# Kernel optimization log

Measured on AMD Instinct MI355X. Metric: run time of the kernel, lower is better.

## Reference

```python
import jax, jax.numpy as jnp
import numpy as np

DT = 0.01
REG = 0.01

def setup_inputs() -> dict:
    key = jax.random.key(0)
    k1, k2, k3, k4 = jax.random.split(key, 4)
    B, C_in, L = 16, 128, 4096
    C_out, KS = 256, 9
    return {
        "x": jax.random.normal(k1, (B, C_in, L), dtype=jnp.float32),
        "weight": jax.random.normal(k2, (C_out, C_in, KS), dtype=jnp.float32) * np.sqrt(2.0 / (C_out * KS)),
        "bias": jnp.zeros((C_out,), dtype=jnp.float32),
        "vel": jax.random.normal(k3, (C_in, KS), dtype=jnp.float32) * 0.1,
        "acc": jax.random.normal(k4, (C_in, KS), dtype=jnp.float32) * 0.01,
        "ks": 9,
        "stride": 1,
        "pad": 4,
    }

def reference(x, weight, bias, vel, acc, ks, stride, pad):
    # x: [B, C_in, L]
    if pad > 0:
        x = jnp.pad(x, ((0, 0), (0, 0), (pad, pad)), mode="edge")  # replicate pad
    L_pad = x.shape[2]
    L_out = (L_pad - ks) // stride + 1
    t_off = jnp.arange(ks, dtype=jnp.float32) * DT  # [ks]
    # unfold: gather sliding windows -> [B, C_in, L_out, ks]
    idx = jnp.arange(L_out)[:, None] * stride + jnp.arange(ks)[None, :]
    xu = x[:, :, idx]
    # per-tap physics offset: vel*t + 0.5*acc*t^2, shape [C_in, ks] broadcast
    offset = vel * t_off + 0.5 * acc * (t_off ** 2)  # [C_in, ks]
    xt = xu + offset[None, :, None, :]  # [B, C_in, L_out, ks]
    # GEMM: [B, L_out, C_in*ks] x [C_in*ks, C_out]
    out = jnp.einsum("bclk,ock->bol", xt, weight) + bias[None, :, None]
    phys = REG * (jnp.mean(vel ** 2) + jnp.mean(acc ** 2))
    return (out, phys)
```

## Files before the change

### kernel.cpp

```cpp
#include <hip/hip_runtime.h>
#include <hip/hip_bf16.h>

typedef unsigned short u16;
typedef __bf16 bf16x8 __attribute__((ext_vector_type(8)));
typedef float f32x4 __attribute__((ext_vector_type(4)));
typedef float f32x16 __attribute__((ext_vector_type(16)));
typedef unsigned short ushort8 __attribute__((ext_vector_type(8)));

#define C_IN   128
#define C_OUT  256
#define BATCH  16
#define LEN    4096
#define KS     9
#define PAD    4
#define LPAD   (LEN + 2*PAD)
#define KTOT   (C_IN * KS)
#define NSTEP  72

#define XT_BLKS    1040
#define W5_BLKS    1152
#define EB_BLKS    256

__device__ inline u16 f2bf(float f) {
    __hip_bfloat16 h = __float2bfloat16(f);
    return __builtin_bit_cast(u16, h);
}

__device__ __forceinline__ void g2l16(const void* g, void* l) {
    __builtin_amdgcn_global_load_lds(
        (const __attribute__((address_space(1))) void*)g,
        (__attribute__((address_space(3))) void*)l, 16, 0, 0);
}

__global__ void prep_all(const float* __restrict__ x, const float* __restrict__ w,
                         const float* __restrict__ bias, const float* __restrict__ vel,
                         const float* __restrict__ acc_in,
                         u16* __restrict__ xt, u16* __restrict__ w5,
                         float* __restrict__ ebias, float* __restrict__ phys_out) {
    int bid = blockIdx.x;
    int t = threadIdx.x;
    if (bid < XT_BLKS) {
        int b    = bid / 65;
        int lblk = bid % 65;
        int lane = t & 63;
        int jb   = t >> 6;
        int lp   = lblk * 64 + lane;
        if (lp >= LPAD) return;
        int l = lp - PAD;
        l = l < 0 ? 0 : (l > LEN - 1 ? LEN - 1 : l);
        const float* xb = x + (size_t)b * C_IN * LEN + l;
        u16* row = xt + ((size_t)b * LPAD + lp) * C_IN;
        int key = lp & 15;
        #pragma unroll
        for (int jj = 0; jj < 4; ++jj) {
            int cblk = jb * 4 + jj;
            ushort8 v;
            #pragma unroll
            for (int e = 0; e < 8; ++e)
                v[e] = f2bf(xb[(size_t)(cblk * 8 + e) * LEN]);
            int jstore = cblk ^ key;
            *reinterpret_cast<ushort8*>(row + jstore * 8) = v;
        }
        return;
    }
    if (bid < XT_BLKS + W5_BLKS) {
        int i = (bid - XT_BLKS) * 256 + t;
        int e    = i & 7;
        int lane = (i >> 3) & 63;
        int g    = (i >> 9) & 7;
        int s    = i >> 12;
        int o    = g * 32 + (lane & 31);
        int hi   = lane >> 5;
        int c    = (s & 7) * 16 + hi * 8 + e;
        int k    = s >> 3;
        w5[i] = f2bf(w[((size_t)o * C_IN + c) * KS + k]);
        return;
    }
    __shared__ float red[256];
    int o = bid - (XT_BLKS + W5_BLKS);
    float sum = 0.f;
    for (int i = t; i < KTOT; i += 256) {
        int k = i % KS;
        float tk = k * 0.01f;
        float off = vel[i] * tk + 0.5f * acc_in[i] * tk * tk;
        sum += off * w[(size_t)o * KTOT + i];
    }
    red[t] = sum;
    __syncthreads();
    for (int h = 128; h > 0; h >>= 1) {
        if (t < h) red[t] += red[t + h];
        __syncthreads();
    }
    if (t == 0) ebias[o] = bias[o] + red[0];

    if (o == 0) {
        __syncthreads();
        float pv = 0.f;
        for (int i = t; i < KTOT; i += 256) {
            float v = vel[i], a = acc_in[i];
            pv += v * v + a * a;
        }
        red[t] = pv;
        __syncthreads();
        for (int h = 128; h > 0; h >>= 1) {
            if (t < h) red[t] += red[t + h];
            __syncthreads();
        }
        if (t == 0) *phys_out = 0.01f * (red[0] / (float)KTOT);
    }
}

__global__ __launch_bounds__(256, 2) void conv_main(const u16* __restrict__ xt,
                                                    const u16* __restrict__ w5,
                                                    const float* __restrict__ ebias,
                                                    float* __restrict__ out) {
    __shared__ u16 ldsx[17408];
    __shared__ u16 ldsa[2][4096];

    int b     = blockIdx.y;
    int lbase = blockIdx.x * 128;
    int t     = threadIdx.x;
    int lane  = t & 63;
    int w     = t >> 6;
    int wm    = w >> 1;
    int wn    = w & 1;
    int l31   = lane & 31;
    int hi    = lane >> 5;

    {
        const u16* bsrc = xt + ((size_t)b * LPAD + lbase) * C_IN;
        #pragma unroll
        for (int j = 0; j < 8; ++j)
            g2l16(bsrc + (j * 256 + t) * 8, ldsx + (j * 256 + w * 64) * 8);
        if (t < 128)
            g2l16(bsrc + (2048 + t) * 8, ldsx + (2048 + w * 64) * 8);
        #pragma unroll
        for (int j = 0; j < 2; ++j)
            g2l16(w5 + (j * 256 + t) * 8, ldsa[0] + (j * 256 + w * 64) * 8);
    }
    asm volatile("s_waitcnt vmcnt(0)" ::: "memory");
    __builtin_amdgcn_s_barrier();

    f32x16 acc[4][2] = {};
    const char* ldsbase = reinterpret_cast<const char*>(ldsx);

    #define LOAD_A(BUF, AF)                                                      \
        {                                                                        \
            const u16* ab_ = ldsa[BUF] + ((wm * 4) * 64 + lane) * 8;             \
            _Pragma("unroll")                                                    \
            for (int mi = 0; mi < 4; ++mi)                                       \
                AF[mi] = *reinterpret_cast<const bf16x8*>(ab_ + mi * 512);       \
        }
    #define LOAD_B(S, BF)                                                        \
        {                                                                        \
            int k_ = (S) >> 3;                                                   \
            int sl_ = ((S) & 7) * 2 + hi;                                        \
            _Pragma("unroll")                                                    \
            for (int nj = 0; nj < 2; ++nj) {                                     \
                int row_  = wn * 64 + nj * 32 + l31 + k_;                        \
                int addr_ = row_ * 256 + ((sl_ ^ (row_ & 15)) << 4);             \
                BF[nj] = *reinterpret_cast<const bf16x8*>(ldsbase + addr_);      \
            }                                                                    \
        }
    #define STAGE_A(S, BUF)                                                      \
        {                                                                        \
            const u16* as_ = w5 + (size_t)(S) * 4096;                            \
            _Pragma("unroll")                                                    \
            for (int j = 0; j < 2; ++j)                                          \
                g2l16(as_ + (j * 256 + t) * 8, ldsa[BUF] + (j * 256 + w * 64) * 8); \
        }
    #define MFMA8(AF, BF)                                                        \
        {                                                                        \
            _Pragma("unroll")                                                    \
            for (int mi = 0; mi < 4; ++mi)                                       \
                _Pragma("unroll")                                                \
                for (int nj = 0; nj < 2; ++nj)                                   \
                    acc[mi][nj] = __builtin_amdgcn_mfma_f32_32x32x16_bf16(       \
                        AF[mi], BF[nj], acc[mi][nj], 0, 0, 0);                   \
        }

    bf16x8 aA[4], aB[4], bA[2], bB[2];
    LOAD_B(0, bA);

    #pragma unroll
    for (int s = 0; s < NSTEP; s += 2) {
        STAGE_A(s + 1, 1);
        LOAD_A(0, aA);
        LOAD_B(s + 1, bB);
        MFMA8(aA, bA);
        asm volatile("s_waitcnt vmcnt(0) lgkmcnt(0)" ::: "memory");
        __builtin_amdgcn_s_barrier();
        if (s + 2 < NSTEP) STAGE_A(s + 2, 0);
        LOAD_A(1, aB);
        if (s + 2 < NSTEP) LOAD_B(s + 2, bA);
        MFMA8(aB, bB);
        if (s + 2 < NSTEP) {
            asm volatile("s_waitcnt vmcnt(0) lgkmcnt(0)" ::: "memory");
            __builtin_amdgcn_s_barrier();
        }
    }

    #pragma unroll
    for (int mi = 0; mi < 4; ++mi) {
        #pragma unroll
        for (int nj = 0; nj < 2; ++nj) {
            int o0 = wm * 128 + mi * 32 + hi * 4;
            int l  = lbase + wn * 64 + nj * 32 + l31;
            #pragma unroll
            for (int q = 0; q < 4; ++q) {
                f32x4 eb = *reinterpret_cast<const f32x4*>(ebias + o0 + q * 8);
                float* op = out + (size_t)(b * C_OUT + o0 + q * 8) * LEN + l;
                #pragma unroll
                for (int p = 0; p < 4; ++p)
                    op[(size_t)p * LEN] = acc[mi][nj][q * 4 + p] + eb[p];
            }
        }
    }
    #undef LOAD_A
    #undef LOAD_B
    #undef STAGE_A
    #undef MFMA8
}

extern "C" void kernel_launch(void* const* d_in, const int* in_sizes, int n_in,
                              void* d_out, int out_size, void* d_ws, size_t ws_size,
                              hipStream_t stream) {
    const float* x      = (const float*)d_in[0];
    const float* weight = (const float*)d_in[1];
    const float* bias   = (const float*)d_in[2];
    const float* vel    = (const float*)d_in[3];
    const float* acc    = (const float*)d_in[4];
    float* out = (float*)d_out;

    char* ws = (char*)d_ws;
    u16*  xt    = (u16*)ws;
    u16*  w5    = (u16*)(ws + (size_t)BATCH * LPAD * C_IN * 2);
    float* ebias = (float*)(ws + (size_t)BATCH * LPAD * C_IN * 2 + (size_t)C_OUT * KTOT * 2);

    hipLaunchKernelGGL(prep_all, dim3(XT_BLKS + W5_BLKS + EB_BLKS), dim3(256), 0, stream,
                       x, weight, bias, vel, acc, xt, w5, ebias,
                       out + (size_t)BATCH * C_OUT * LEN);
    hipLaunchKernelGGL(conv_main, dim3(LEN / 128, BATCH), dim3(256), 0, stream,
                       xt, w5, ebias, out);
}
```

Baseline: 62.78 us.

## Deepen weight staging to four LDS buffers with partial vmcnt waits

Replaces the double-buffered weight tile pipeline with a four-slot ring buffer that prefetches three steps ahead. Barriers now wait with vmcnt(2) instead of draining all global loads. Fragment loads are issued one step earlier, and the MFMA blocks are wrapped in s_setprio. The aim is to hide global-to-LDS latency behind MFMA work. In exchange, LDS use grows by about 18 KB per block, which may limit occupancy at 2 blocks per CU. The vmcnt(2) accounting has to match the number of outstanding loads exactly, or the kernel will read stale data.

```diff
diff --git a/kernel.cpp b/kernel.cpp
--- a/kernel.cpp
+++ b/kernel.cpp
@@ -114,8 +114,8 @@
                                                     const u16* __restrict__ w5,
                                                     const float* __restrict__ ebias,
                                                     float* __restrict__ out) {
-    __shared__ u16 ldsx[17408];
-    __shared__ u16 ldsa[2][4096];
+    __shared__ u16 ldsx[18432];
+    __shared__ u16 ldsa[4][4096];
 
     int b     = blockIdx.y;
     int lbase = blockIdx.x * 128;
@@ -130,15 +130,16 @@
     {
         const u16* bsrc = xt + ((size_t)b * LPAD + lbase) * C_IN;
         #pragma unroll
-        for (int j = 0; j < 8; ++j)
+        for (int j = 0; j < 9; ++j)
             g2l16(bsrc + (j * 256 + t) * 8, ldsx + (j * 256 + w * 64) * 8);
-        if (t < 128)
-            g2l16(bsrc + (2048 + t) * 8, ldsx + (2048 + w * 64) * 8);
-        #pragma unroll
-        for (int j = 0; j < 2; ++j)
-            g2l16(w5 + (j * 256 + t) * 8, ldsa[0] + (j * 256 + w * 64) * 8);
-    }
-    asm volatile("s_waitcnt vmcnt(0)" ::: "memory");
+        #pragma unroll
+        for (int p = 0; p < 3; ++p)
+            #pragma unroll
+            for (int j = 0; j < 2; ++j)
+                g2l16(w5 + (size_t)p * 4096 + (j * 256 + t) * 8,
+                      ldsa[p] + (j * 256 + w * 64) * 8);
+    }
+    asm volatile("s_waitcnt vmcnt(2)" ::: "memory");
     __builtin_amdgcn_s_barrier();
 
     f32x16 acc[4][2] = {};
@@ -162,12 +163,13 @@
                 BF[nj] = *reinterpret_cast<const bf16x8*>(ldsbase + addr_);      \
             }                                                                    \
         }
-    #define STAGE_A(S, BUF)                                                      \
+    #define STAGE_A(S)                                                           \
         {                                                                        \
             const u16* as_ = w5 + (size_t)(S) * 4096;                            \
+            u16* ad_ = ldsa[(S) & 3];                                            \
             _Pragma("unroll")                                                    \
             for (int j = 0; j < 2; ++j)                                          \
-                g2l16(as_ + (j * 256 + t) * 8, ldsa[BUF] + (j * 256 + w * 64) * 8); \
+                g2l16(as_ + (j * 256 + t) * 8, ad_ + (j * 256 + w * 64) * 8);    \
         }
     #define MFMA8(AF, BF)                                                        \
         {                                                                        \
@@ -178,26 +180,32 @@
                     acc[mi][nj] = __builtin_amdgcn_mfma_f32_32x32x16_bf16(       \
                         AF[mi], BF[nj], acc[mi][nj], 0, 0, 0);                   \
         }
+    #define ENDSTEP(E)                                                           \
+        {                                                                        \
+            if ((E) + 3 < NSTEP) asm volatile("s_waitcnt vmcnt(2)" ::: "memory");\
+            else                 asm volatile("s_waitcnt vmcnt(0)" ::: "memory");\
+            __builtin_amdgcn_s_barrier();                                        \
+        }
 
     bf16x8 aA[4], aB[4], bA[2], bB[2];
+    LOAD_A(0, aA);
     LOAD_B(0, bA);
 
     #pragma unroll
     for (int s = 0; s < NSTEP; s += 2) {
-        STAGE_A(s + 1, 1);
-        LOAD_A(0, aA);
+        if (s + 3 < NSTEP) STAGE_A(s + 3);
+        LOAD_A((s + 1) & 3, aB);
         LOAD_B(s + 1, bB);
+        __builtin_amdgcn_s_setprio(1);
         MFMA8(aA, bA);
-        asm volatile("s_waitcnt vmcnt(0) lgkmcnt(0)" ::: "memory");
-        __builtin_amdgcn_s_barrier();
-        if (s + 2 < NSTEP) STAGE_A(s + 2, 0);
-        LOAD_A(1, aB);
-        if (s + 2 < NSTEP) LOAD_B(s + 2, bA);
+        __builtin_amdgcn_s_setprio(0);
+        ENDSTEP(s);
+        if (s + 4 < NSTEP) STAGE_A(s + 4);
+        if (s + 2 < NSTEP) { LOAD_A((s + 2) & 3, aA); LOAD_B(s + 2, bA); }
+        __builtin_amdgcn_s_setprio(1);
         MFMA8(aB, bB);
-        if (s + 2 < NSTEP) {
-            asm volatile("s_waitcnt vmcnt(0) lgkmcnt(0)" ::: "memory");
-            __builtin_amdgcn_s_barrier();
-        }
+        __builtin_amdgcn_s_setprio(0);
+        if (s + 2 < NSTEP) ENDSTEP(s + 1);
     }
 
     #pragma unroll
@@ -220,6 +228,7 @@
     #undef LOAD_B
     #undef STAGE_A
     #undef MFMA8
+    #undef ENDSTEP
 }
 
 extern "C" void kernel_launch(void* const* d_in, const int* in_sizes, int n_in,
```

After: 64.36 us. 2.5% more time.

## Load weight fragments directly from global and use two-wave blocks with larger tiles

Applied to the files above, without the earlier changes.

The conv GEMM now runs with 128 threads (two waves) per block. Each wave computes a 128x128 tile with a 4x4 MFMA accumulator grid, up from 4x2. Weight fragments are read straight from global memory into registers with register double buffering, replacing the LDS weight staging and the per-step barriers. This drops synchronisation and LDS traffic but doubles accumulator registers, halves the waves per block, and exposes global-load latency on the weight operand.

```diff
diff --git a/kernel.cpp b/kernel.cpp
--- a/kernel.cpp
+++ b/kernel.cpp
@@ -110,102 +110,80 @@
     }
 }
 
-__global__ __launch_bounds__(256, 2) void conv_main(const u16* __restrict__ xt,
+__global__ __launch_bounds__(128, 1) void conv_main(const u16* __restrict__ xt,
                                                     const u16* __restrict__ w5,
                                                     const float* __restrict__ ebias,
                                                     float* __restrict__ out) {
     __shared__ u16 ldsx[17408];
-    __shared__ u16 ldsa[2][4096];
 
     int b     = blockIdx.y;
     int lbase = blockIdx.x * 128;
     int t     = threadIdx.x;
     int lane  = t & 63;
-    int w     = t >> 6;
-    int wm    = w >> 1;
-    int wn    = w & 1;
+    int wm    = t >> 6;
     int l31   = lane & 31;
     int hi    = lane >> 5;
 
-    {
-        const u16* bsrc = xt + ((size_t)b * LPAD + lbase) * C_IN;
-        #pragma unroll
-        for (int j = 0; j < 8; ++j)
-            g2l16(bsrc + (j * 256 + t) * 8, ldsx + (j * 256 + w * 64) * 8);
-        if (t < 128)
-            g2l16(bsrc + (2048 + t) * 8, ldsx + (2048 + w * 64) * 8);
-        #pragma unroll
-        for (int j = 0; j < 2; ++j)
-            g2l16(w5 + (j * 256 + t) * 8, ldsa[0] + (j * 256 + w * 64) * 8);
-    }
-    asm volatile("s_waitcnt vmcnt(0)" ::: "memory");
-    __builtin_amdgcn_s_barrier();
-
-    f32x16 acc[4][2] = {};
-    const char* ldsbase = reinterpret_cast<const char*>(ldsx);
-
-    #define LOAD_A(BUF, AF)                                                      \
+    const u16* alane = w5 + ((size_t)(wm * 4) * 64 + lane) * 8;
+
+    #define LOAD_A(S, AF)                                                        \
         {                                                                        \
-            const u16* ab_ = ldsa[BUF] + ((wm * 4) * 64 + lane) * 8;             \
+            const u16* p_ = alane + (size_t)(S) * 4096;                          \
             _Pragma("unroll")                                                    \
             for (int mi = 0; mi < 4; ++mi)                                       \
-                AF[mi] = *reinterpret_cast<const bf16x8*>(ab_ + mi * 512);       \
+                AF[mi] = *reinterpret_cast<const bf16x8*>(p_ + mi * 512);        \
         }
     #define LOAD_B(S, BF)                                                        \
         {                                                                        \
             int k_ = (S) >> 3;                                                   \
             int sl_ = ((S) & 7) * 2 + hi;                                        \
             _Pragma("unroll")                                                    \
-            for (int nj = 0; nj < 2; ++nj) {                                     \
-                int row_  = wn * 64 + nj * 32 + l31 + k_;                        \
+            for (int nj = 0; nj < 4; ++nj) {                                     \
+                int row_  = nj * 32 + l31 + k_;                                  \
                 int addr_ = row_ * 256 + ((sl_ ^ (row_ & 15)) << 4);             \
                 BF[nj] = *reinterpret_cast<const bf16x8*>(ldsbase + addr_);      \
             }                                                                    \
         }
-    #define STAGE_A(S, BUF)                                                      \
-        {                                                                        \
-            const u16* as_ = w5 + (size_t)(S) * 4096;                            \
-            _Pragma("unroll")                                                    \
-            for (int j = 0; j < 2; ++j)                                          \
-                g2l16(as_ + (j * 256 + t) * 8, ldsa[BUF] + (j * 256 + w * 64) * 8); \
-        }
-    #define MFMA8(AF, BF)                                                        \
+    #define MFMA16(AF, BF)                                                       \
         {                                                                        \
             _Pragma("unroll")                                                    \
             for (int mi = 0; mi < 4; ++mi)                                       \
                 _Pragma("unroll")                                                \
-                for (int nj = 0; nj < 2; ++nj)                                   \
+                for (int nj = 0; nj < 4; ++nj)                                   \
                     acc[mi][nj] = __builtin_amdgcn_mfma_f32_32x32x16_bf16(       \
                         AF[mi], BF[nj], acc[mi][nj], 0, 0, 0);                   \
         }
 
-    bf16x8 aA[4], aB[4], bA[2], bB[2];
+    bf16x8 aA[4], aB[4], bA[4], bB[4];
+
+    {
+        const u16* bsrc = xt + ((size_t)b * LPAD + lbase) * C_IN;
+        #pragma unroll
+        for (int j = 0; j < 17; ++j)
+            g2l16(bsrc + (j * 128 + t) * 8, ldsx + (j * 128 + wm * 64) * 8);
+    }
+    LOAD_A(0, aA);
+    __syncthreads();
+
+    f32x16 acc[4][4] = {};
+    const char* ldsbase = reinterpret_cast<const char*>(ldsx);
     LOAD_B(0, bA);
 
     #pragma unroll
     for (int s = 0; s < NSTEP; s += 2) {
-        STAGE_A(s + 1, 1);
-        LOAD_A(0, aA);
+        LOAD_A(s + 1, aB);
         LOAD_B(s + 1, bB);
-        MFMA8(aA, bA);
-        asm volatile("s_waitcnt vmcnt(0) lgkmcnt(0)" ::: "memory");
-        __builtin_amdgcn_s_barrier();
-        if (s + 2 < NSTEP) STAGE_A(s + 2, 0);
-        LOAD_A(1, aB);
-        if (s + 2 < NSTEP) LOAD_B(s + 2, bA);
-        MFMA8(aB, bB);
-        if (s + 2 < NSTEP) {
-            asm volatile("s_waitcnt vmcnt(0) lgkmcnt(0)" ::: "memory");
-            __builtin_amdgcn_s_barrier();
-        }
+        MFMA16(aA, bA);
+        if (s + 2 < NSTEP) { LOAD_A(s + 2, aA); LOAD_B(s + 2, bA); }
+        MFMA16(aB, bB);
     }
 
     #pragma unroll
     for (int mi = 0; mi < 4; ++mi) {
+        int o0 = wm * 128 + mi * 32 + hi * 4;
         #pragma unroll
-        for (int nj = 0; nj < 2; ++nj) {
-            int o0 = wm * 128 + mi * 32 + hi * 4;
-            int l  = lbase + wn * 64 + nj * 32 + l31;
+        for (int nj = 0; nj < 4; ++nj) {
+            int l = lbase + nj * 32 + l31;
             #pragma unroll
             for (int q = 0; q < 4; ++q) {
                 f32x4 eb = *reinterpret_cast<const f32x4*>(ebias + o0 + q * 8);
@@ -218,8 +196,7 @@
     }
     #undef LOAD_A
     #undef LOAD_B
-    #undef STAGE_A
-    #undef MFMA8
+    #undef MFMA16
 }
 
 extern "C" void kernel_launch(void* const* d_in, const int* in_sizes, int n_in,
@@ -240,6 +217,6 @@
     hipLaunchKernelGGL(prep_all, dim3(XT_BLKS + W5_BLKS + EB_BLKS), dim3(256), 0, stream,
                        x, weight, bias, vel, acc, xt, w5, ebias,
                        out + (size_t)BATCH * C_OUT * LEN);
-    hipLaunchKernelGGL(conv_main, dim3(LEN / 128, BATCH), dim3(256), 0, stream,
+    hipLaunchKernelGGL(conv_main, dim3(LEN / 128, BATCH), dim3(128), 0, stream,
                        xt, w5, ebias, out);
 }
```

Result: faster. 57.64 us (-8.2%).
